# Optimization experiments

Hardware: AMD Instinct MI355X
Metric: run time of the kernel (lower is better)

The kernel has to match this reference:

```python
import jax, jax.numpy as jnp
import numpy as np

N_HRU, N_CH, N_GW = 100000, 40000, 60000
E = 250000          # edges per relation
D = 256             # node feature dim (== hidden_channels so layers stack)
H = 256             # hidden_channels
B = 64              # number of graphs in the batch
TD = 32             # train_input_dim
OUT = 16            # out_channels
L = 2               # num_layers
R = 5               # relations: 0=sw_gw, 1=hydrograph, 2=sw, 3=gw_sw, 4=self_loop


def setup_inputs() -> dict:
    key = jax.random.key(0)
    ks = jax.random.split(key, 32)
    inp = {}
    inp["x_hru"] = jax.random.normal(ks[0], (N_HRU, D), jnp.float32)
    inp["x_channel"] = jax.random.normal(ks[1], (N_CH, D), jnp.float32)
    inp["x_gw"] = jax.random.normal(ks[2], (N_GW, D), jnp.float32)
    rels = [("swgw", N_HRU, N_GW), ("hyd", N_CH, N_CH), ("sw", N_HRU, N_CH),
            ("gwsw", N_GW, N_CH), ("slf", N_HRU, N_HRU)]
    i = 3
    for nm, ns, nd in rels:
        inp[f"src_{nm}"] = jax.random.randint(ks[i], (E,), 0, ns, jnp.int32); i += 1
        inp[f"dst_{nm}"] = jax.random.randint(ks[i], (E,), 0, nd, jnp.int32); i += 1
    inp["batch"] = jnp.sort(jax.random.randint(ks[i], (N_CH,), 0, B, jnp.int32)); i += 1
    inp["train_data"] = jax.random.normal(ks[i], (B, TD), jnp.float32); i += 1
    s = 1.0 / np.sqrt(D)
    inp["Wl"] = jax.random.normal(ks[i], (L, R, D, H), jnp.float32) * s; i += 1   # neighbor lin
    inp["Wr"] = jax.random.normal(ks[i], (L, R, D, H), jnp.float32) * s; i += 1   # root lin
    inp["bsage"] = jnp.zeros((L, R, H), jnp.float32)
    inp["fc1_w"] = jax.random.normal(ks[i], (H + TD, 128), jnp.float32) / np.sqrt(H + TD); i += 1
    inp["fc1_b"] = jnp.zeros((128,), jnp.float32)
    inp["fc2_w"] = jax.random.normal(ks[i], (128, OUT), jnp.float32) / np.sqrt(128.0); i += 1
    inp["fc2_b"] = jnp.zeros((OUT,), jnp.float32)
    return inp


def _sage(x_src, x_dst, src, dst, n_dst, Wl, Wr, b):
    # PyG SAGEConv: lin_l(mean_j x_j) + lin_r(x_dst); bias only in lin_l.
    msg = x_src[src]                                                    # [E, D] gather
    agg = jax.ops.segment_sum(msg, dst, num_segments=n_dst)            # [n_dst, D]
    cnt = jax.ops.segment_sum(jnp.ones((dst.shape[0],), x_src.dtype), dst, num_segments=n_dst)
    agg = agg / jnp.maximum(cnt, 1.0)[:, None]                          # mean (0 for isolated)
    return agg @ Wl + b + x_dst @ Wr


def reference(x_hru, x_channel, x_gw,
              src_swgw, dst_swgw, src_hyd, dst_hyd, src_sw, dst_sw,
              src_gwsw, dst_gwsw, src_slf, dst_slf,
              batch, train_data, Wl, Wr, bsage, fc1_w, fc1_b, fc2_w, fc2_b):
    h, c, g = x_hru, x_channel, x_gw
    for l in range(L):
        out_gw = _sage(h, g, src_swgw, dst_swgw, N_GW, Wl[l, 0], Wr[l, 0], bsage[l, 0])
        o1 = _sage(c, c, src_hyd, dst_hyd, N_CH, Wl[l, 1], Wr[l, 1], bsage[l, 1])
        o2 = _sage(h, c, src_sw, dst_sw, N_CH, Wl[l, 2], Wr[l, 2], bsage[l, 2])
        o3 = _sage(g, c, src_gwsw, dst_gwsw, N_CH, Wl[l, 3], Wr[l, 3], bsage[l, 3])
        out_ch = (o1 + o2 + o3) / 3.0                                   # HeteroConv aggr='mean'
        out_hru = _sage(h, h, src_slf, dst_slf, N_HRU, Wl[l, 4], Wr[l, 4], bsage[l, 4])
        h, c, g = jax.nn.relu(out_hru), jax.nn.relu(out_ch), jax.nn.relu(out_gw)
    pooled = jax.ops.segment_sum(c, batch, num_segments=B)              # global_mean_pool on channel
    cnt = jax.ops.segment_sum(jnp.ones((N_CH,), c.dtype), batch, num_segments=B)
    pooled = pooled / jnp.maximum(cnt, 1.0)[:, None]                    # [B, H]
    x = jnp.concatenate([pooled, train_data], axis=1)                   # [B, H+TD]
    x = jax.nn.relu(x @ fc1_w + fc1_b)
    return x @ fc2_w + fc2_b                                            # [B, OUT]
```

## Files before the change

kernel.cpp:

```cpp
#include <hip/hip_runtime.h>

#define E_EDGES 250000
#define NHRU 100000
#define NCH  40000
#define NGW  60000
#define NCNT 280000
#define NBLK_SCAN 1094

#define NB_E    977
#define NB_CNT  (5 * NB_E)
#define NB_CVT  25000
#define NB_PREP 3076

typedef __attribute__((ext_vector_type(4))) float f32x4;
typedef __attribute__((ext_vector_type(2))) float f32x2;
typedef __attribute__((ext_vector_type(8))) __bf16 bf16x8;
typedef __attribute__((ext_vector_type(8))) short short8;

__device__ __forceinline__ float bf2f(short h) {
  unsigned u = ((unsigned)(unsigned short)h) << 16;
  return __builtin_bit_cast(float, u);
}
__device__ __forceinline__ short f2bf(float f) {
  unsigned u = __builtin_bit_cast(unsigned, f);
  u = u + 0x7fffu + ((u >> 16) & 1u);
  return (short)(u >> 16);
}

__device__ __forceinline__ void load_lds16(const void* g, void* lds) {
  __builtin_amdgcn_global_load_lds(
      (const __attribute__((address_space(1))) unsigned*)g,
      (__attribute__((address_space(3))) unsigned*)lds, 16, 0, 0);
}

struct P5 { const int* p[5]; };

__global__ void fused_pre(const float* __restrict__ xh, const float* __restrict__ xc,
                          const float* __restrict__ xg, short* __restrict__ oh,
                          short* __restrict__ oc, short* __restrict__ og,
                          const float* __restrict__ Wl, const float* __restrict__ Wr,
                          const float* __restrict__ bs, short* __restrict__ Bt,
                          float* __restrict__ bias,
                          P5 dst, int* __restrict__ cnt, int* __restrict__ rank) {
  int b = blockIdx.x;
  if (b < NB_CNT) {
    const int COFF[5] = {0, 60000, 100000, 140000, 180000};
    int r = b / NB_E;
    int e = (b - r * NB_E) * 256 + threadIdx.x;
    if (e < E_EDGES) {
      int d = dst.p[r][e];
      int rk = atomicAdd(&cnt[COFF[r] + d], 1);
      rank[r * E_EDGES + e] = rk;
    }
  } else if (b < NB_CNT + NB_CVT) {
    int i = (b - NB_CNT) * 256 + threadIdx.x;
    const int n1 = NHRU * 32, n2 = n1 + NCH * 32;
    const float* in; short* out; int j;
    if (i < n1) { in = xh; out = oh; j = i; }
    else if (i < n2) { in = xc; out = oc; j = i - n1; }
    else { in = xg; out = og; j = i - n2; }
    const f32x4* p = reinterpret_cast<const f32x4*>(in) + (size_t)j * 2;
    f32x4 v0 = __builtin_nontemporal_load(p);
    f32x4 v1 = __builtin_nontemporal_load(p + 1);
    short8 o;
#pragma unroll
    for (int k = 0; k < 4; ++k) { o[k] = f2bf(v0[k]); o[4 + k] = f2bf(v1[k]); }
    reinterpret_cast<short8*>(out)[j] = o;
  } else {
    int i = (b - NB_CNT - NB_CVT) * 256 + threadIdx.x;
    const float inv3 = 1.0f / 3.0f;
    if (i < 131072) {
      int n = i >> 9, k = i & 511;
      float v = (k < 256) ? Wl[(0 * 256 + k) * 256 + n]
                          : Wr[(0 * 256 + (k - 256)) * 256 + n];
      Bt[i] = f2bf(v);
    } else if (i < 393216) {
      int j = i - 131072;
      int n = j >> 10, k = j & 1023;
      float v;
      if (k < 768) {
        int r = 1 + (k >> 8), kk = k & 255;
        v = Wl[((0 * 5 + r) * 256 + kk) * 256 + n] * inv3;
      } else {
        int kk = k - 768;
        v = (Wr[((0 * 5 + 1) * 256 + kk) * 256 + n] +
             Wr[((0 * 5 + 2) * 256 + kk) * 256 + n] +
             Wr[((0 * 5 + 3) * 256 + kk) * 256 + n]) * inv3;
      }
      Bt[i] = f2bf(v);
    } else if (i < 524288) {
      int j = i - 393216;
      int n = j >> 9, k = j & 511;
      float v = (k < 256) ? Wl[((0 * 5 + 4) * 256 + k) * 256 + n]
                          : Wr[((0 * 5 + 4) * 256 + (k - 256)) * 256 + n];
      Bt[i] = f2bf(v);
    } else if (i < 786432) {
      int j = i - 524288;
      int n = j >> 10, k = j & 1023;
      float v;
      if (k < 768) {
        int r = 1 + (k >> 8), kk = k & 255;
        v = Wl[((5 + r) * 256 + kk) * 256 + n] * inv3;
      } else {
        int kk = k - 768;
        v = (Wr[((5 + 1) * 256 + kk) * 256 + n] +
             Wr[((5 + 2) * 256 + kk) * 256 + n] +
             Wr[((5 + 3) * 256 + kk) * 256 + n]) * inv3;
      }
      Bt[i] = f2bf(v);
    } else if (i < 787456) {
      int j = i - 786432;
      int g = j >> 8, n = j & 255;
      float v;
      if (g == 0)      v = bs[n];
      else if (g == 1) v = (bs[256 + n] + bs[512 + n] + bs[768 + n]) * inv3;
      else if (g == 2) v = bs[1024 + n];
      else             v = (bs[1280 + 256 + n] + bs[1280 + 512 + n] + bs[1280 + 768 + n]) * inv3;
      bias[j] = v;
    }
  }
}

__global__ void scan_a(const int* __restrict__ cnt, int* __restrict__ bsum) {
  int i = blockIdx.x * 256 + threadIdx.x;
  int v = (i < NCNT) ? cnt[i] : 0;
  int lane = threadIdx.x & 63, wv = threadIdx.x >> 6;
  for (int d = 1; d < 64; d <<= 1) v += __shfl_down(v, d);
  __shared__ int ws[4];
  if (lane == 0) ws[wv] = v;
  __syncthreads();
  if (threadIdx.x == 0) bsum[blockIdx.x] = ws[0] + ws[1] + ws[2] + ws[3];
}

__global__ void scan_b(const int* __restrict__ bsum, int* __restrict__ boff) {
  int t = threadIdx.x;
  int e0 = 2 * t, e1 = 2 * t + 1;
  int v0 = (e0 < NBLK_SCAN) ? bsum[e0] : 0;
  int v1 = (e1 < NBLK_SCAN) ? bsum[e1] : 0;
  __shared__ int lds[1024];
  lds[t] = v0 + v1;
  __syncthreads();
  for (int o = 1; o < 1024; o <<= 1) {
    int add = (t >= o) ? lds[t - o] : 0;
    __syncthreads();
    lds[t] += add;
    __syncthreads();
  }
  int ex = (t == 0) ? 0 : lds[t - 1];
  if (e0 < NBLK_SCAN) boff[e0] = ex;
  if (e1 < NBLK_SCAN) boff[e1] = ex + v0;
}

__global__ void scan_c(const int* __restrict__ cnt, const int* __restrict__ boff,
                       int* __restrict__ S) {
  int i = blockIdx.x * 256 + threadIdx.x;
  int v = (i < NCNT) ? cnt[i] : 0;
  int lane = threadIdx.x & 63, wv = threadIdx.x >> 6;
  int inc = v;
  for (int d = 1; d < 64; d <<= 1) {
    int y = __shfl_up(inc, d);
    if (lane >= d) inc += y;
  }
  __shared__ int ws[4];
  if (lane == 63) ws[wv] = inc;
  __syncthreads();
  int wex = 0;
  for (int k = 0; k < 4; ++k) wex += (k < wv) ? ws[k] : 0;
  int ex = boff[blockIdx.x] + wex + inc - v;
  if (i < NCNT) S[i] = ex;
  if (blockIdx.x == 0 && threadIdx.x == 0) S[NCNT] = 5 * E_EDGES;
}

__global__ void scatter_kernel(P5 src, P5 dst, const int* __restrict__ rp,
                               const int* __restrict__ rank, int* __restrict__ ssrc) {
  const int COFF[5] = {0, 60000, 100000, 140000, 180000};
  int r = blockIdx.y;
  int e = blockIdx.x * blockDim.x + threadIdx.x;
  if (e < E_EDGES) {
    int d = dst.p[r][e];
    int idx = rp[COFF[r] + d] + rank[r * E_EDGES + e];
    ssrc[idx] = src.p[r][e];
  }
}

struct AggTab { const short* src[5]; short* out[5]; };

__global__ void agg_pair(const int* __restrict__ rp, const int* __restrict__ ssrc,
                         AggTab tab, int be0, int be1, int be2,
                         int r0, int r1, int r2, int r3) {
  int b = blockIdx.x;
  int r, b0;
  if (b < be0)      { r = r0; b0 = 0; }
  else if (b < be1) { r = r1; b0 = be0; }
  else if (b < be2) { r = r2; b0 = be1; }
  else              { r = r3; b0 = be2; }
  int coff = r == 0 ? 0 : r == 1 ? 60000 : r == 2 ? 100000 : r == 3 ? 140000 : 180000;
  int nrel = r == 0 ? 60000 : r == 4 ? 100000 : 40000;
  const short* xs = r == 0 ? tab.src[0] : r == 1 ? tab.src[1] : r == 2 ? tab.src[2]
                   : r == 3 ? tab.src[3] : tab.src[4];
  short* ob = r == 0 ? tab.out[0] : r == 1 ? tab.out[1] : r == 2 ? tab.out[2]
             : r == 3 ? tab.out[3] : tab.out[4];

  int wid = threadIdx.x >> 6;
  int lane = threadIdx.x & 63;
  int half = lane >> 5, l32 = lane & 31;
  int row = (b - b0) * 8 + wid * 2 + half;
  bool active = row < nrel;
  int item = coff + row;
  int lo = 0, hi = 0;
  if (active) { lo = rp[item]; hi = rp[item + 1]; }

  f32x2 a0[4], a1[4];
#pragma unroll
  for (int k = 0; k < 4; ++k) { a0[k] = (f32x2){0.f, 0.f}; a1[k] = (f32x2){0.f, 0.f}; }
  int e = lo;
  for (; e + 1 < hi; e += 2) {
    int s0 = ssrc[e];
    int s1 = ssrc[e + 1];
    uint4 u0 = *reinterpret_cast<const uint4*>(xs + (size_t)s0 * 256 + l32 * 8);
    uint4 u1 = *reinterpret_cast<const uint4*>(xs + (size_t)s1 * 256 + l32 * 8);
    unsigned d0[4] = {u0.x, u0.y, u0.z, u0.w};
    unsigned d1[4] = {u1.x, u1.y, u1.z, u1.w};
#pragma unroll
    for (int k = 0; k < 4; ++k) {
      a0[k] += (f32x2){__builtin_bit_cast(float, d0[k] << 16),
                       __builtin_bit_cast(float, d0[k] & 0xffff0000u)};
      a1[k] += (f32x2){__builtin_bit_cast(float, d1[k] << 16),
                       __builtin_bit_cast(float, d1[k] & 0xffff0000u)};
    }
  }
  if (e < hi) {
    int s = ssrc[e];
    uint4 u = *reinterpret_cast<const uint4*>(xs + (size_t)s * 256 + l32 * 8);
    unsigned d[4] = {u.x, u.y, u.z, u.w};
#pragma unroll
    for (int k = 0; k < 4; ++k) {
      a0[k] += (f32x2){__builtin_bit_cast(float, d[k] << 16),
                       __builtin_bit_cast(float, d[k] & 0xffff0000u)};
    }
  }
#pragma unroll
  for (int k = 0; k < 4; ++k) a0[k] += a1[k];
  if (active) {
    int c = hi - lo; if (c < 1) c = 1;
    float inv = 1.0f / (float)c;
    short8 o;
#pragma unroll
    for (int k = 0; k < 4; ++k) {
      o[2 * k] = f2bf(a0[k].x * inv);
      o[2 * k + 1] = f2bf(a0[k].y * inv);
    }
    *reinterpret_cast<short8*>(ob + (size_t)row * 256 + l32 * 8) = o;
  }
}

struct Srcs4 { const short* s[4]; };
struct GArgs {
  Srcs4 srcs; const short* Bt; const float* bias;
  int M; int K; short* outb; float* outf;
};

__device__ __forceinline__ void gemm_body(const GArgs& a, int bx) {
  __shared__ short sm[24576];
  short* Asm = sm;
  short* Bsm = sm + 8192;
  const int tid = threadIdx.x;
  const int lane = tid & 63;
  const int w = tid >> 6;
  const int wr = w >> 2, wc = w & 3;
  const int m0 = bx * 128;
  const int M = a.M, K = a.K;

  f32x4 acc[4][4];
#pragma unroll
  for (int i = 0; i < 4; ++i)
#pragma unroll
    for (int j = 0; j < 4; ++j) acc[i][j] = (f32x4){0.f, 0.f, 0.f, 0.f};

  for (int k0 = 0; k0 < K; k0 += 64) {
    const short* Aq = a.srcs.s[k0 >> 8];
    const int kc = k0 & 255;
#pragma unroll
    for (int rr = 0; rr < 2; ++rr) {
      const int rbase = w * 16 + rr * 8;
      const int row = rbase + (lane >> 3);
      const int cs = ((lane & 7) ^ (row & 7)) << 3;
      int gr = m0 + row; gr = gr < M ? gr : M - 1;
      load_lds16(Aq + (size_t)gr * 256 + kc + cs, &Asm[rbase * 64]);
    }
#pragma unroll
    for (int rr = 0; rr < 4; ++rr) {
      const int rbase = w * 32 + rr * 8;
      const int row = rbase + (lane >> 3);
      const int cs = ((lane & 7) ^ (row & 7)) << 3;
      load_lds16(a.Bt + (size_t)row * K + k0 + cs, &Bsm[rbase * 64]);
    }
    __syncthreads();
#pragma unroll
    for (int h = 0; h < 2; ++h) {
      const int cg = (h << 2) + (lane >> 4);
      bf16x8 af[4], bfr[4];
#pragma unroll
      for (int mi = 0; mi < 4; ++mi) {
        const int r = wr * 64 + mi * 16 + (lane & 15);
        af[mi] = *reinterpret_cast<const bf16x8*>(&Asm[r * 64 + ((cg ^ (r & 7)) << 3)]);
      }
#pragma unroll
      for (int nj = 0; nj < 4; ++nj) {
        const int r = wc * 64 + nj * 16 + (lane & 15);
        bfr[nj] = *reinterpret_cast<const bf16x8*>(&Bsm[r * 64 + ((cg ^ (r & 7)) << 3)]);
      }
#pragma unroll
      for (int mi = 0; mi < 4; ++mi)
#pragma unroll
        for (int nj = 0; nj < 4; ++nj)
          acc[mi][nj] = __builtin_amdgcn_mfma_f32_16x16x32_bf16(af[mi], bfr[nj], acc[mi][nj], 0, 0, 0);
    }
    __syncthreads();
  }

  const int rb = (lane >> 4) << 2;
  const int cl = lane & 15;

  if (a.outb) {
#pragma unroll
    for (int halfp = 0; halfp < 2; ++halfp) {
      __syncthreads();
      if (wr == halfp) {
#pragma unroll
        for (int mi = 0; mi < 4; ++mi)
#pragma unroll
          for (int nj = 0; nj < 4; ++nj) {
            const int col = wc * 64 + nj * 16 + cl;
            const float bv = a.bias[col];
#pragma unroll
            for (int j = 0; j < 4; ++j) {
              const int rloc = mi * 16 + rb + j;
              float v = fmaxf(acc[mi][nj][j] + bv, 0.0f);
              sm[rloc * 264 + col] = f2bf(v);
            }
          }
      }
      __syncthreads();
#pragma unroll
      for (int q = 0; q < 4; ++q) {
        int c = q * 512 + tid;
        int rloc = c >> 5;
        int coff = (c & 31) * 8;
        int grow = m0 + halfp * 64 + rloc;
        if (grow < M) {
          short8 vv = *reinterpret_cast<const short8*>(&sm[rloc * 264 + coff]);
          *reinterpret_cast<short8*>(a.outb + (size_t)grow * 256 + coff) = vv;
        }
      }
    }
  }
  if (a.outf) {
    float* fsm = reinterpret_cast<float*>(sm);
#pragma unroll
    for (int p = 0; p < 4; ++p) {
      __syncthreads();
      if (wr == (p >> 1)) {
#pragma unroll
        for (int mm = 0; mm < 2; ++mm) {
          const int mi = (p & 1) * 2 + mm;
#pragma unroll
          for (int nj = 0; nj < 4; ++nj) {
            const int col = wc * 64 + nj * 16 + cl;
            const float bv = a.bias[col];
#pragma unroll
            for (int j = 0; j < 4; ++j) {
              const int rloc = mi * 16 + rb + j - (p & 1) * 32;
              float v = fmaxf(acc[mi][nj][j] + bv, 0.0f);
              fsm[rloc * 260 + col] = v;
            }
          }
        }
      }
      __syncthreads();
#pragma unroll
      for (int q = 0; q < 4; ++q) {
        int c = q * 512 + tid;
        int rloc = c >> 6;
        int coff = (c & 63) * 4;
        int grow = m0 + p * 32 + rloc;
        if (grow < M) {
          float4 vv = *reinterpret_cast<const float4*>(&fsm[rloc * 260 + coff]);
          *reinterpret_cast<float4*>(a.outf + (size_t)grow * 256 + coff) = vv;
        }
      }
    }
  }
}

__global__ __launch_bounds__(512) void gemm_bt(GArgs a) {
  gemm_body(a, blockIdx.x);
}

__global__ __launch_bounds__(512) void gemm_multi3(GArgs a0, GArgs a1, GArgs a2,
                                                   int nb0, int nb01) {
  int bx = blockIdx.x;
  if (bx < nb0) gemm_body(a0, bx);
  else if (bx < nb01) gemm_body(a1, bx - nb0);
  else gemm_body(a2, bx - nb01);
}

__device__ __forceinline__ int lower_bound(const int* a, int n, int v) {
  int lo = 0, hi = n;
  while (lo < hi) { int mid = (lo + hi) >> 1; if (a[mid] < v) lo = mid + 1; else hi = mid; }
  return lo;
}

__global__ void pool_partial(const float* __restrict__ c2, const int* __restrict__ batch,
                             float* __restrict__ pooled_sum) {
  int r0 = blockIdx.x * 64;
  int t = threadIdx.x;
  float acc = 0.f;
  int prevb = batch[r0];
  for (int i = 0; i < 64; ++i) {
    int r = r0 + i;
    int b = batch[r];
    if (b != prevb) {
      atomicAdd(&pooled_sum[prevb * 256 + t], acc);
      acc = 0.f; prevb = b;
    }
    acc += c2[(size_t)r * 256 + t];
  }
  atomicAdd(&pooled_sum[prevb * 256 + t], acc);
}

__global__ void mlp_kernel(const float* __restrict__ pooled_sum, const int* __restrict__ batch,
                           const float* __restrict__ train,
                           const float* __restrict__ fc1w, const float* __restrict__ fc1b,
                           const float* __restrict__ fc2w, const float* __restrict__ fc2b,
                           float* __restrict__ out) {
  int b = blockIdx.x, t = threadIdx.x;
  __shared__ float x[288];
  __shared__ float hsm[128];
  __shared__ float sinv;
  if (t == 0) {
    int lo = lower_bound(batch, NCH, b);
    int hi = lower_bound(batch, NCH, b + 1);
    int c = hi - lo; if (c < 1) c = 1;
    sinv = 1.0f / (float)c;
  }
  __syncthreads();
  float inv = sinv;
  x[t] = pooled_sum[b * 256 + t] * inv;
  x[128 + t] = pooled_sum[b * 256 + 128 + t] * inv;
  if (t < 32) x[256 + t] = train[b * 32 + t];
  __syncthreads();
  float s = fc1b[t];
  for (int i = 0; i < 288; ++i) s += x[i] * fc1w[i * 128 + t];
  hsm[t] = fmaxf(s, 0.f);
  __syncthreads();
  if (t < 16) {
    float o = fc2b[t];
    for (int i = 0; i < 128; ++i) o += hsm[i] * fc2w[i * 16 + t];
    out[b * 16 + t] = o;
  }
}

extern "C" void kernel_launch(void* const* d_in, const int* in_sizes, int n_in,
                              void* d_out, int out_size, void* d_ws, size_t ws_size,
                              hipStream_t stream) {
  const float* x_hru = (const float*)d_in[0];
  const float* x_ch  = (const float*)d_in[1];
  const float* x_gw  = (const float*)d_in[2];
  const int* src_swgw = (const int*)d_in[3];
  const int* dst_swgw = (const int*)d_in[4];
  const int* src_hyd  = (const int*)d_in[5];
  const int* dst_hyd  = (const int*)d_in[6];
  const int* src_sw   = (const int*)d_in[7];
  const int* dst_sw   = (const int*)d_in[8];
  const int* src_gwsw = (const int*)d_in[9];
  const int* dst_gwsw = (const int*)d_in[10];
  const int* src_slf  = (const int*)d_in[11];
  const int* dst_slf  = (const int*)d_in[12];
  const int* batch    = (const int*)d_in[13];
  const float* train  = (const float*)d_in[14];
  const float* Wl     = (const float*)d_in[15];
  const float* Wr     = (const float*)d_in[16];
  const float* bs     = (const float*)d_in[17];
  const float* fc1w   = (const float*)d_in[18];
  const float* fc1b   = (const float*)d_in[19];
  const float* fc2w   = (const float*)d_in[20];
  const float* fc2b   = (const float*)d_in[21];
  float* out = (float*)d_out;

  char* ws = (char*)d_ws;
  size_t off = 0;
  auto alloc = [&](size_t bytes) -> void* {
    off = (off + 255) & ~(size_t)255;
    void* p = ws + off;
    off += bytes;
    return p;
  };

  short* xb0h = (short*)alloc((size_t)NHRU * 256 * 2);
  short* xb0c = (short*)alloc((size_t)NCH * 256 * 2);
  short* xb0g = (short*)alloc((size_t)NGW * 256 * 2);
  short* xb1h = (short*)alloc((size_t)NHRU * 256 * 2);
  short* xb1c = (short*)alloc((size_t)NCH * 256 * 2);
  short* xb1g = (short*)alloc((size_t)NGW * 256 * 2);
  short* agg_gw  = (short*)alloc((size_t)NGW * 256 * 2);
  short* agg_c0  = (short*)alloc((size_t)NCH * 256 * 2);
  short* agg_c1  = (short*)alloc((size_t)NCH * 256 * 2);
  short* agg_c2  = (short*)alloc((size_t)NCH * 256 * 2);
  short* agg_hru = (short*)alloc((size_t)NHRU * 256 * 2);
  float* c2f = (float*)alloc((size_t)NCH * 256 * 4);
  int* cnt  = (int*)alloc(NCNT * 4);
  int* rp   = (int*)alloc((NCNT + 1) * 4);
  int* rank = (int*)alloc((size_t)5 * E_EDGES * 4);
  int* bsum = (int*)alloc(NBLK_SCAN * 4);
  int* boff = (int*)alloc(NBLK_SCAN * 4);
  int* ssrc = (int*)alloc((size_t)5 * E_EDGES * 4);
  short* BtBuf = (short*)alloc(786432 * 2);
  float* biasBuf = (float*)alloc(1024 * 4);
  float* pooled_sum = (float*)alloc(64 * 256 * 4);

  hipMemsetAsync(cnt, 0, NCNT * 4, stream);
  hipMemsetAsync(pooled_sum, 0, 64 * 256 * 4, stream);

  P5 dsts; dsts.p[0] = dst_swgw; dsts.p[1] = dst_hyd; dsts.p[2] = dst_sw;
  dsts.p[3] = dst_gwsw; dsts.p[4] = dst_slf;
  P5 srcs; srcs.p[0] = src_swgw; srcs.p[1] = src_hyd; srcs.p[2] = src_sw;
  srcs.p[3] = src_gwsw; srcs.p[4] = src_slf;

  fused_pre<<<NB_CNT + NB_CVT + NB_PREP, 256, 0, stream>>>(
      x_hru, x_ch, x_gw, xb0h, xb0c, xb0g,
      Wl, Wr, bs, BtBuf, biasBuf, dsts, cnt, rank);

  scan_a<<<NBLK_SCAN, 256, 0, stream>>>(cnt, bsum);
  scan_b<<<1, 1024, 0, stream>>>(bsum, boff);
  scan_c<<<NBLK_SCAN, 256, 0, stream>>>(cnt, boff, rp);
  dim3 eg(NB_E, 5);
  scatter_kernel<<<eg, 256, 0, stream>>>(srcs, dsts, rp, rank, ssrc);

  AggTab t0{};
  t0.src[0] = xb0h; t0.out[0] = agg_gw;
  t0.src[1] = xb0c; t0.out[1] = agg_c0;
  t0.src[2] = xb0h; t0.out[2] = agg_c1;
  t0.src[3] = xb0g; t0.out[3] = agg_c2;
  t0.src[4] = xb0h; t0.out[4] = agg_hru;

  agg_pair<<<25000, 256, 0, stream>>>(rp, ssrc, t0, 7500, 12500, 25000, 0, 2, 4, 4);
  agg_pair<<<10000, 256, 0, stream>>>(rp, ssrc, t0, 5000, 10000, 10000, 1, 3, 3, 3);

  {
    GArgs g0{}, g1{}, g2{};
    g0.srcs.s[0] = agg_c0; g0.srcs.s[1] = agg_c1; g0.srcs.s[2] = agg_c2; g0.srcs.s[3] = xb0c;
    g0.Bt = BtBuf + 131072; g0.bias = biasBuf + 256; g0.M = NCH; g0.K = 1024;
    g0.outb = xb1c; g0.outf = nullptr;
    g1.srcs.s[0] = agg_gw; g1.srcs.s[1] = xb0g;
    g1.Bt = BtBuf + 0; g1.bias = biasBuf + 0; g1.M = NGW; g1.K = 512;
    g1.outb = xb1g; g1.outf = nullptr;
    g2.srcs.s[0] = agg_hru; g2.srcs.s[1] = xb0h;
    g2.Bt = BtBuf + 393216; g2.bias = biasBuf + 512; g2.M = NHRU; g2.K = 512;
    g2.outb = xb1h; g2.outf = nullptr;
    const int nb0 = (NCH + 127) / 128;
    const int nb1 = (NGW + 127) / 128;
    const int nb2 = (NHRU + 127) / 128;
    gemm_multi3<<<dim3(nb0 + nb1 + nb2), 512, 0, stream>>>(g0, g1, g2, nb0, nb0 + nb1);
  }

  AggTab t1{};
  t1.src[1] = xb1c; t1.out[1] = agg_c0;
  t1.src[2] = xb1h; t1.out[2] = agg_c1;
  t1.src[3] = xb1g; t1.out[3] = agg_c2;

  agg_pair<<<5000, 256, 0, stream>>>(rp, ssrc, t1, 5000, 5000, 5000, 2, 2, 2, 2);
  agg_pair<<<10000, 256, 0, stream>>>(rp, ssrc, t1, 5000, 10000, 10000, 1, 3, 3, 3);

  {
    GArgs g{};
    g.srcs.s[0] = agg_c0; g.srcs.s[1] = agg_c1; g.srcs.s[2] = agg_c2; g.srcs.s[3] = xb1c;
    g.Bt = BtBuf + 524288; g.bias = biasBuf + 768; g.M = NCH; g.K = 1024;
    g.outb = nullptr; g.outf = c2f;
    gemm_bt<<<dim3((NCH + 127) / 128), 512, 0, stream>>>(g);
  }

  pool_partial<<<625, 256, 0, stream>>>(c2f, batch, pooled_sum);
  mlp_kernel<<<64, 128, 0, stream>>>(pooled_sum, batch, train, fc1w, fc1b, fc2w, fc2b, out);

  (void)in_sizes; (void)n_in; (void)out_size; (void)ws_size;
}
```

Baseline: 495.2 us.

## Double-buffer GEMM K-loop with 32-wide tiles and merge aggregation launches

The GEMM main loop moves from single-buffered 64-wide K tiles to double-buffered 32-wide tiles, so the next tile's global-to-LDS loads are issued while MFMAs run on the current one, and there is one barrier per step. The separate agg_pair launches for each layer are merged into one launch per layer by adding a fifth relation range. This is meant to hide load latency in the GEMM and cut launch gaps and tail effects in aggregation. In exchange the GEMM runs twice as many iterations with less work per barrier.

```diff
diff --git a/kernel.cpp b/kernel.cpp
--- a/kernel.cpp
+++ b/kernel.cpp
@@ -186,14 +186,15 @@
 struct AggTab { const short* src[5]; short* out[5]; };
 
 __global__ void agg_pair(const int* __restrict__ rp, const int* __restrict__ ssrc,
-                         AggTab tab, int be0, int be1, int be2,
-                         int r0, int r1, int r2, int r3) {
+                         AggTab tab, int be0, int be1, int be2, int be3,
+                         int r0, int r1, int r2, int r3, int r4) {
   int b = blockIdx.x;
   int r, b0;
   if (b < be0)      { r = r0; b0 = 0; }
   else if (b < be1) { r = r1; b0 = be0; }
   else if (b < be2) { r = r2; b0 = be1; }
-  else              { r = r3; b0 = be2; }
+  else if (b < be3) { r = r3; b0 = be2; }
+  else              { r = r4; b0 = be3; }
   int coff = r == 0 ? 0 : r == 1 ? 60000 : r == 2 ? 100000 : r == 3 ? 140000 : 180000;
   int nrel = r == 0 ? 60000 : r == 4 ? 100000 : 40000;
   const short* xs = r == 0 ? tab.src[0] : r == 1 ? tab.src[1] : r == 2 ? tab.src[2]
@@ -260,10 +261,31 @@
   int M; int K; short* outb; float* outf;
 };
 
+__device__ __forceinline__ void gemm_stage(const GArgs& a, short* sm, int m0,
+                                           int k0, int sel, int w, int lane) {
+  short* Abuf = sm + sel * 12288;
+  short* Bbuf = sm + sel * 12288 + 4096;
+  const short* Aq = a.srcs.s[k0 >> 8];
+  const int kc = k0 & 255;
+  const int M = a.M;
+  {
+    const int rbase = w * 16;
+    const int row = rbase + (lane >> 2);
+    const int cs = ((lane & 3) ^ (row & 3)) << 3;
+    int gr = m0 + row; gr = gr < M ? gr : M - 1;
+    load_lds16(Aq + (size_t)gr * 256 + kc + cs, &Abuf[rbase * 32]);
+  }
+#pragma unroll
+  for (int rr = 0; rr < 2; ++rr) {
+    const int rbase = w * 32 + rr * 16;
+    const int row = rbase + (lane >> 2);
+    const int cs = ((lane & 3) ^ (row & 3)) << 3;
+    load_lds16(a.Bt + (size_t)row * a.K + k0 + cs, &Bbuf[rbase * 32]);
+  }
+}
+
 __device__ __forceinline__ void gemm_body(const GArgs& a, int bx) {
   __shared__ short sm[24576];
-  short* Asm = sm;
-  short* Bsm = sm + 8192;
   const int tid = threadIdx.x;
   const int lane = tid & 63;
   const int w = tid >> 6;
@@ -277,38 +299,26 @@
 #pragma unroll
     for (int j = 0; j < 4; ++j) acc[i][j] = (f32x4){0.f, 0.f, 0.f, 0.f};
 
-  for (int k0 = 0; k0 < K; k0 += 64) {
-    const short* Aq = a.srcs.s[k0 >> 8];
-    const int kc = k0 & 255;
-#pragma unroll
-    for (int rr = 0; rr < 2; ++rr) {
-      const int rbase = w * 16 + rr * 8;
-      const int row = rbase + (lane >> 3);
-      const int cs = ((lane & 7) ^ (row & 7)) << 3;
-      int gr = m0 + row; gr = gr < M ? gr : M - 1;
-      load_lds16(Aq + (size_t)gr * 256 + kc + cs, &Asm[rbase * 64]);
-    }
-#pragma unroll
-    for (int rr = 0; rr < 4; ++rr) {
-      const int rbase = w * 32 + rr * 8;
-      const int row = rbase + (lane >> 3);
-      const int cs = ((lane & 7) ^ (row & 7)) << 3;
-      load_lds16(a.Bt + (size_t)row * K + k0 + cs, &Bsm[rbase * 64]);
-    }
-    __syncthreads();
-#pragma unroll
-    for (int h = 0; h < 2; ++h) {
-      const int cg = (h << 2) + (lane >> 4);
+  const int nt = K >> 5;
+  gemm_stage(a, sm, m0, 0, 0, w, lane);
+  __syncthreads();
+  int sel = 0;
+  for (int t = 0; t < nt; ++t) {
+    if (t + 1 < nt) gemm_stage(a, sm, m0, (t + 1) << 5, sel ^ 1, w, lane);
+    {
+      const short* Abuf = sm + sel * 12288;
+      const short* Bbuf = sm + sel * 12288 + 4096;
+      const int cg = lane >> 4;
       bf16x8 af[4], bfr[4];
 #pragma unroll
       for (int mi = 0; mi < 4; ++mi) {
         const int r = wr * 64 + mi * 16 + (lane & 15);
-        af[mi] = *reinterpret_cast<const bf16x8*>(&Asm[r * 64 + ((cg ^ (r & 7)) << 3)]);
+        af[mi] = *reinterpret_cast<const bf16x8*>(&Abuf[r * 32 + ((cg ^ (r & 3)) << 3)]);
       }
 #pragma unroll
       for (int nj = 0; nj < 4; ++nj) {
         const int r = wc * 64 + nj * 16 + (lane & 15);
-        bfr[nj] = *reinterpret_cast<const bf16x8*>(&Bsm[r * 64 + ((cg ^ (r & 7)) << 3)]);
+        bfr[nj] = *reinterpret_cast<const bf16x8*>(&Bbuf[r * 32 + ((cg ^ (r & 3)) << 3)]);
       }
 #pragma unroll
       for (int mi = 0; mi < 4; ++mi)
@@ -317,6 +327,7 @@
           acc[mi][nj] = __builtin_amdgcn_mfma_f32_16x16x32_bf16(af[mi], bfr[nj], acc[mi][nj], 0, 0, 0);
     }
     __syncthreads();
+    sel ^= 1;
   }
 
   const int rb = (lane >> 4) << 2;
@@ -537,15 +548,15 @@
   dim3 eg(NB_E, 5);
   scatter_kernel<<<eg, 256, 0, stream>>>(srcs, dsts, rp, rank, ssrc);
 
-  AggTab t0{};
-  t0.src[0] = xb0h; t0.out[0] = agg_gw;
-  t0.src[1] = xb0c; t0.out[1] = agg_c0;
-  t0.src[2] = xb0h; t0.out[2] = agg_c1;
-  t0.src[3] = xb0g; t0.out[3] = agg_c2;
-  t0.src[4] = xb0h; t0.out[4] = agg_hru;
-
-  agg_pair<<<25000, 256, 0, stream>>>(rp, ssrc, t0, 7500, 12500, 25000, 0, 2, 4, 4);
-  agg_pair<<<10000, 256, 0, stream>>>(rp, ssrc, t0, 5000, 10000, 10000, 1, 3, 3, 3);
+  {
+    AggTab t0{};
+    t0.src[0] = xb0h; t0.out[0] = agg_gw;
+    t0.src[1] = xb0c; t0.out[1] = agg_c0;
+    t0.src[2] = xb0h; t0.out[2] = agg_c1;
+    t0.src[3] = xb0g; t0.out[3] = agg_c2;
+    t0.src[4] = xb0h; t0.out[4] = agg_hru;
+    agg_pair<<<35000, 256, 0, stream>>>(rp, ssrc, t0, 7500, 12500, 17500, 22500, 0, 1, 2, 3, 4);
+  }
 
   {
     GArgs g0{}, g1{}, g2{};
@@ -564,13 +575,13 @@
     gemm_multi3<<<dim3(nb0 + nb1 + nb2), 512, 0, stream>>>(g0, g1, g2, nb0, nb0 + nb1);
   }
 
-  AggTab t1{};
-  t1.src[1] = xb1c; t1.out[1] = agg_c0;
-  t1.src[2] = xb1h; t1.out[2] = agg_c1;
-  t1.src[3] = xb1g; t1.out[3] = agg_c2;
-
-  agg_pair<<<5000, 256, 0, stream>>>(rp, ssrc, t1, 5000, 5000, 5000, 2, 2, 2, 2);
-  agg_pair<<<10000, 256, 0, stream>>>(rp, ssrc, t1, 5000, 10000, 10000, 1, 3, 3, 3);
+  {
+    AggTab t1{};
+    t1.src[1] = xb1c; t1.out[1] = agg_c0;
+    t1.src[2] = xb1h; t1.out[2] = agg_c1;
+    t1.src[3] = xb1g; t1.out[3] = agg_c2;
+    agg_pair<<<15000, 256, 0, stream>>>(rp, ssrc, t1, 5000, 10000, 15000, 15000, 1, 2, 3, 3, 3);
+  }
 
   {
     GArgs g{};
```

After: 485.8 us. Within noise of the previous version (-1.9%).
